# Performance work log

Hardware: AMD Instinct MI355X
Metric: run time of the kernel (lower is better)

Reference implementation:

```python
import jax, jax.numpy as jnp
import numpy as np
import math

HEAD_DIM = 128
N_HEADS = 32
N_KV_HEADS = 8
ROPE_THETA = 10000.0


def _rotate_half(x):
    x1, x2 = jnp.split(x, 2, axis=-1)
    return jnp.concatenate([-x2, x1], axis=-1)


def _rope_cos_sin(position_ids, head_dim, theta):
    # position_ids: [B, S] int
    inv_freq = 1.0 / (theta ** (jnp.arange(0, head_dim, 2, dtype=jnp.float32) / head_dim))
    freqs = position_ids.astype(jnp.float32)[..., None] * inv_freq[None, None, :]  # [B,S,D/2]
    emb = jnp.concatenate([freqs, freqs], axis=-1)  # [B,S,D]
    return jnp.cos(emb), jnp.sin(emb)


def setup_inputs() -> dict:
    key = jax.random.key(0)
    k1, k2, k3, k4, k5 = jax.random.split(key, 5)
    B, S, H = 1, 2048, 4096
    hidden_states = jax.random.normal(k1, (B, S, H), dtype=jnp.float32)
    Wq = jax.random.normal(k2, (N_HEADS * HEAD_DIM, H), dtype=jnp.float32) * (1.0 / math.sqrt(H))
    Wk = jax.random.normal(k3, (N_KV_HEADS * HEAD_DIM, H), dtype=jnp.float32) * (1.0 / math.sqrt(H))
    Wv = jax.random.normal(k4, (N_KV_HEADS * HEAD_DIM, H), dtype=jnp.float32) * (1.0 / math.sqrt(H))
    Wo = jax.random.normal(k5, (H, N_HEADS * HEAD_DIM), dtype=jnp.float32) * (1.0 / math.sqrt(H))
    position_ids = jnp.arange(S, dtype=jnp.int32)[None, :]
    return {"hidden_states": hidden_states, "Wq": Wq, "Wk": Wk, "Wv": Wv, "Wo": Wo,
            "position_ids": position_ids}


def reference(hidden_states, Wq, Wk, Wv, Wo, position_ids):
    B, S, H = hidden_states.shape
    d = HEAD_DIM
    groups = N_HEADS // N_KV_HEADS

    # projections (torch Linear: x @ W^T)
    q = (hidden_states @ Wq.T).reshape(B, S, N_HEADS, d).transpose(0, 2, 1, 3)      # [B,Hq,S,d]
    k = (hidden_states @ Wk.T).reshape(B, S, N_KV_HEADS, d).transpose(0, 2, 1, 3)   # [B,Hk,S,d]
    v = (hidden_states @ Wv.T).reshape(B, S, N_KV_HEADS, d).transpose(0, 2, 1, 3)

    cos, sin = _rope_cos_sin(position_ids, d, ROPE_THETA)  # [B,S,d]
    cos = cos[:, None, :, :]
    sin = sin[:, None, :, :]
    q = q * cos + _rotate_half(q) * sin
    k = k * cos + _rotate_half(k) * sin

    # GQA: repeat kv heads
    k = jnp.repeat(k, groups, axis=1)  # [B,Hq,S,d]
    v = jnp.repeat(v, groups, axis=1)

    scores = jnp.einsum('bhqd,bhkd->bhqk', q, k) / math.sqrt(d)
    causal = jnp.tril(jnp.ones((S, S), dtype=bool))
    scores = jnp.where(causal[None, None], scores, jnp.finfo(jnp.float32).min)
    attn = jax.nn.softmax(scores.astype(jnp.float32), axis=-1).astype(q.dtype)

    out = jnp.einsum('bhqk,bhkd->bhqd', attn, v)        # [B,Hq,S,d]
    out = out.transpose(0, 2, 1, 3).reshape(B, S, N_HEADS * d)
    return out @ Wo.T
```

## Files before the change

### kernel.cpp

```cpp
#include <hip/hip_runtime.h>
#include <hip/hip_bf16.h>
#include <cstdint>
#include <cstddef>

#define S_LEN 2048
#define HID   4096
#define HD    128
#define NH    32
#define NKV   8
#define KVW   (NKV * HD)
#define QKVN  (HID + 2 * KVW)

typedef __bf16 bf16x8_t __attribute__((ext_vector_type(8)));
typedef float  f32x4_t  __attribute__((ext_vector_type(4)));
typedef unsigned short u16x8_t __attribute__((ext_vector_type(8)));

__device__ __forceinline__ unsigned short f2b(float f) {
  unsigned u = __float_as_uint(f);
  u += 0x7FFFu + ((u >> 16) & 1u);
  return (unsigned short)(u >> 16);
}
__device__ __forceinline__ float b2f(unsigned short v) {
  return __uint_as_float(((unsigned)v) << 16);
}
__device__ __forceinline__ void gld_lds16(const void* g, void* l) {
  __builtin_amdgcn_global_load_lds(
      (const __attribute__((address_space(1))) void*)g,
      (__attribute__((address_space(3))) void*)l, 16, 0, 0);
}

__global__ void cvt_kernel(const float* __restrict__ src,
                           unsigned short* __restrict__ dst, int n4) {
  int i = blockIdx.x * blockDim.x + threadIdx.x;
  int stride = gridDim.x * blockDim.x;
  for (; i < n4; i += stride) {
    float4 v = reinterpret_cast<const float4*>(src)[i];
    ushort4 o;
    o.x = f2b(v.x); o.y = f2b(v.y); o.z = f2b(v.z); o.w = f2b(v.w);
    reinterpret_cast<ushort4*>(dst)[i] = o;
  }
}

__global__ void rope_kernel(unsigned short* __restrict__ Q,
                            unsigned short* __restrict__ Kb,
                            const int* __restrict__ pos_ids) {
  const int total = S_LEN * (NH + NKV) * 64;
  int idx = blockIdx.x * blockDim.x + threadIdx.x;
  int stride = gridDim.x * blockDim.x;
  for (; idx < total; idx += stride) {
    int s   = idx / ((NH + NKV) * 64);
    int rem = idx % ((NH + NKV) * 64);
    int hp  = rem >> 6;
    int i   = rem & 63;
    unsigned short* ptr; int W, h;
    if (hp < NH) { ptr = Q;  W = HID; h = hp; }
    else         { ptr = Kb; W = KVW; h = hp - NH; }
    float pos = (float)pos_ids[s];
    float ang = pos * __expf(-(float)i * 0.14391156516f);
    float sn, cs;
    sincosf(ang, &sn, &cs);
    size_t base = (size_t)s * W + (size_t)h * HD + i;
    float lo = b2f(ptr[base]);
    float hi = b2f(ptr[base + 64]);
    ptr[base]      = f2b(lo * cs - hi * sn);
    ptr[base + 64] = f2b(hi * cs + lo * sn);
  }
}

template <int BN, int MODE>
__global__ __launch_bounds__(512, 4) void gemm4p_kernel(
    const unsigned short* __restrict__ A, const unsigned short* __restrict__ B,
    void* __restrict__ C0, void* __restrict__ C1, void* __restrict__ C2,
    int N, int K) {
  constexpr int NFR = BN / 64;
  constexpr int ABYTES = 128 * 128;
  constexpr int TILE_LDS = ABYTES + BN * 128;
  __shared__ char ldsB[2 * TILE_LDS];

  const int tid  = threadIdx.x;
  const int lane = tid & 63;
  const int wid  = tid >> 6;
  const int wm = wid >> 2, wn = wid & 3;
  const int lr = lane & 15, g = lane >> 4;
  const int bm = blockIdx.y * 128;
  const int bn = blockIdx.x * BN;
  const int nk = K >> 6;
  const int ni = nk >> 1;
  const int xr = (lr & 7) << 4;

  auto stage_u = [&](int t, int u) {
    if (t >= nk) return;
    const int riu = tid >> 3;
    const int cbs = ((tid & 7) << 4) ^ ((riu & 7) << 4);
    const char* src;
    if (u < 2)
      src = (const char*)A + ((size_t)(bm + u * 64 + riu) * K + t * 64) * 2 + cbs;
    else
      src = (const char*)B + ((size_t)(bn + (u - 2) * 64 + riu) * K + t * 64) * 2 + cbs;
    gld_lds16(src, ldsB + (t & 1) * TILE_LDS + u * 8192 + tid * 16);
  };

  auto rdA = [&](const char* bb, int m, int k) {
    const int row = wm * 64 + m * 16 + lr;
    return *(const bf16x8_t*)(bb + row * 128 + ((k * 64 + g * 16) ^ xr));
  };
  auto rdB = [&](const char* bb, int n, int k) {
    const int row = wn * (BN / 4) + n * 16 + lr;
    return *(const bf16x8_t*)(bb + ABYTES + row * 128 + ((k * 64 + g * 16) ^ xr));
  };

  for (int t = 0; t < 2; ++t)
    for (int u = 0; u < 2 + NFR; ++u) stage_u(t, u);
  asm volatile("s_waitcnt vmcnt(0)" ::: "memory");
  __builtin_amdgcn_sched_barrier(0);
  __builtin_amdgcn_s_barrier();

  f32x4_t acc[4][NFR];
#pragma unroll
  for (int m = 0; m < 4; ++m)
#pragma unroll
    for (int n = 0; n < NFR; ++n) acc[m][n] = f32x4_t{0.f, 0.f, 0.f, 0.f};

  bf16x8_t bfr[NFR][2], af[2][2];

#define MFMA_BLOCK(MB)                                                        \
  __builtin_amdgcn_s_setprio(1);                                              \
  _Pragma("unroll") for (int m = 0; m < 2; ++m)                               \
    _Pragma("unroll") for (int n = 0; n < NFR; ++n)                           \
      _Pragma("unroll") for (int k = 0; k < 2; ++k)                           \
        acc[(MB) + m][n] = __builtin_amdgcn_mfma_f32_16x16x32_bf16(           \
            af[m][k], bfr[n][k], acc[(MB) + m][n], 0, 0, 0);                  \
  __builtin_amdgcn_s_setprio(0);

#define GATE()                                                                \
  __builtin_amdgcn_s_barrier();                                               \
  asm volatile("s_waitcnt lgkmcnt(0)" ::: "memory");                          \
  __builtin_amdgcn_sched_barrier(0);

#define RD_A2(bb, m0)                                                         \
  _Pragma("unroll") for (int m = 0; m < 2; ++m)                               \
    _Pragma("unroll") for (int k = 0; k < 2; ++k)                             \
      af[m][k] = rdA(bb, (m0) + m, k);

#define RD_B(bb)                                                              \
  _Pragma("unroll") for (int n = 0; n < NFR; ++n)                             \
    _Pragma("unroll") for (int k = 0; k < 2; ++k)                             \
      bfr[n][k] = rdB(bb, n, k);

  for (int i = 0; i < ni; ++i) {
    const char* bE = ldsB;
    const char* bO = ldsB + TILE_LDS;
    const int tO = 2 * i + 1, tE2 = 2 * i + 2, tO2 = 2 * i + 3;
    const bool last = (i == ni - 1);

    RD_B(bE);
    RD_A2(bE, 0);
    if (i > 0) { stage_u(tO, 0); stage_u(tO, 1); }
    GATE(); MFMA_BLOCK(0);
    __builtin_amdgcn_s_barrier();

    RD_A2(bE, 2);
#pragma unroll
    for (int u = 0; u < NFR; ++u) stage_u(tE2, 2 + u);
    GATE(); MFMA_BLOCK(2);
    if (last) { asm volatile("s_waitcnt vmcnt(0)" ::: "memory"); }
    else      { asm volatile("s_waitcnt vmcnt(%0)" :: "n"(NFR) : "memory"); }
    __builtin_amdgcn_sched_barrier(0);
    __builtin_amdgcn_s_barrier();

    RD_B(bO);
    RD_A2(bO, 0);
    stage_u(tE2, 0); stage_u(tE2, 1);
    GATE(); MFMA_BLOCK(0);
    __builtin_amdgcn_s_barrier();

    RD_A2(bO, 2);
#pragma unroll
    for (int u = 0; u < NFR; ++u) stage_u(tO2, 2 + u);
    GATE(); MFMA_BLOCK(2);
    if (!last) { asm volatile("s_waitcnt vmcnt(%0)" :: "n"(NFR) : "memory"); }
    __builtin_amdgcn_sched_barrier(0);
    __builtin_amdgcn_s_barrier();
  }
#undef MFMA_BLOCK
#undef GATE
#undef RD_A2
#undef RD_B

#pragma unroll
  for (int mf = 0; mf < 4; ++mf) {
    const int row0 = bm + wm * 64 + mf * 16 + g * 4;
#pragma unroll
    for (int nf = 0; nf < NFR; ++nf) {
      const int col = bn + wn * (BN / 4) + nf * 16 + lr;
      if constexpr (MODE == 1) {
#pragma unroll
        for (int r = 0; r < 4; ++r)
          ((float*)C0)[(size_t)(row0 + r) * N + col] = acc[mf][nf][r];
      } else {
        if (col < HID) {
#pragma unroll
          for (int r = 0; r < 4; ++r)
            ((unsigned short*)C0)[(size_t)(row0 + r) * HID + col] = f2b(acc[mf][nf][r]);
        } else if (col < HID + KVW) {
#pragma unroll
          for (int r = 0; r < 4; ++r)
            ((unsigned short*)C1)[(size_t)(row0 + r) * KVW + (col - HID)] = f2b(acc[mf][nf][r]);
        } else {
          const int c2 = col - HID - KVW;
          ushort4 w;
          w.x = f2b(acc[mf][nf][0]); w.y = f2b(acc[mf][nf][1]);
          w.z = f2b(acc[mf][nf][2]); w.w = f2b(acc[mf][nf][3]);
          *(ushort4*)(void*)&((unsigned short*)C2)[(size_t)c2 * S_LEN + row0] = w;
        }
      }
    }
  }
}

__global__ __launch_bounds__(256) void attn_kernel(
    const unsigned short* __restrict__ Q, const unsigned short* __restrict__ K,
    const unsigned short* __restrict__ VtG, unsigned short* __restrict__ O) {
  __shared__ unsigned short Kl[64][136];
  __shared__ unsigned short Vt[128][72];
  __shared__ unsigned short Pl[4][16][72];

  const int tid  = threadIdx.x;
  const int lane = tid & 63;
  const int wave = tid >> 6;
  const int h    = blockIdx.y;
  const int kvh  = h >> 2;
  const int pair = blockIdx.x;
  const int lr   = lane & 15;
  const int g    = lane >> 4;
  const int lk8  = g * 8;
  const float scale = 0.08838834764831845f;
  const unsigned short* Vbase = VtG + (size_t)kvh * HD * S_LEN;

  const int ksr = tid >> 4, ksc = (tid & 15) * 8;
  const int vsr = tid >> 3, vsc = (tid & 7) * 8;

  for (int pass = 0; pass < 2; ++pass) {
    const int qb = pass == 0 ? (31 - pair) : pair;
    const int q0 = qb * 64;
    const int qrow = q0 + wave * 16;
    const int nkv = qb + 1;

    bf16x8_t qf[4];
    {
      const unsigned short* qp = Q + (size_t)(qrow + lr) * HID + (size_t)h * HD;
#pragma unroll
      for (int c = 0; c < 4; ++c)
        qf[c] = *(const bf16x8_t*)(const void*)(qp + c * 32 + lk8);
    }
    f32x4_t oacc[8];
#pragma unroll
    for (int c = 0; c < 8; ++c) oacc[c] = f32x4_t{0.f, 0.f, 0.f, 0.f};
    float m_run = -3e38f, l_run = 0.f;

    u16x8_t kr[4], vr[4];
#pragma unroll
    for (int i = 0; i < 4; ++i)
      kr[i] = *(const u16x8_t*)(const void*)(K + (size_t)(ksr + i * 16) * KVW +
                                             (size_t)kvh * HD + ksc);
#pragma unroll
    for (int i = 0; i < 4; ++i)
      vr[i] = *(const u16x8_t*)(const void*)(Vbase + (size_t)(vsr + i * 32) * S_LEN + vsc);

    for (int it = 0; it < nkv; ++it) {
      const int kv0 = it * 64;
      __builtin_amdgcn_s_barrier();
#pragma unroll
      for (int i = 0; i < 4; ++i)
        *(u16x8_t*)(void*)&Kl[ksr + i * 16][ksc] = kr[i];
#pragma unroll
      for (int i = 0; i < 4; ++i)
        *(u16x8_t*)(void*)&Vt[vsr + i * 32][vsc] = vr[i];
      if (it + 1 < nkv) {
        const int kn = kv0 + 64;
#pragma unroll
        for (int i = 0; i < 4; ++i)
          kr[i] = *(const u16x8_t*)(const void*)(K + (size_t)(kn + ksr + i * 16) * KVW +
                                                 (size_t)kvh * HD + ksc);
#pragma unroll
        for (int i = 0; i < 4; ++i)
          vr[i] = *(const u16x8_t*)(const void*)(Vbase + (size_t)(vsr + i * 32) * S_LEN +
                                                 kn + vsc);
      }
      asm volatile("s_waitcnt lgkmcnt(0)" ::: "memory");
      __builtin_amdgcn_sched_barrier(0);
      __builtin_amdgcn_s_barrier();

      f32x4_t sacc[4];
#pragma unroll
      for (int n = 0; n < 4; ++n) sacc[n] = f32x4_t{0.f, 0.f, 0.f, 0.f};
#pragma unroll
      for (int c = 0; c < 4; ++c) {
        bf16x8_t qc = qf[c];
#pragma unroll
        for (int n = 0; n < 4; ++n) {
          bf16x8_t kf = *(const bf16x8_t*)(const void*)&Kl[n * 16 + lr][c * 32 + lk8];
          sacc[n] = __builtin_amdgcn_mfma_f32_16x16x32_bf16(kf, qc, sacc[n], 0, 0, 0);
        }
      }

      const int qg = qrow + lr;
      const bool diag = (it == nkv - 1);
      float p[16];
      float mloc = -3e38f;
#pragma unroll
      for (int n = 0; n < 4; ++n)
#pragma unroll
        for (int r = 0; r < 4; ++r) {
          float x = sacc[n][r] * scale;
          if (diag) {
            int kg = kv0 + n * 16 + g * 4 + r;
            if (kg > qg) x = -3e38f;
          }
          p[n * 4 + r] = x;
          mloc = fmaxf(mloc, x);
        }
      mloc = fmaxf(mloc, __shfl_xor(mloc, 16));
      mloc = fmaxf(mloc, __shfl_xor(mloc, 32));

      if (__any(mloc > m_run + 8.f)) {
        float m_new = fmaxf(m_run, mloc);
        float alpha = __expf(m_run - m_new);
        float a4[4];
#pragma unroll
        for (int r = 0; r < 4; ++r) a4[r] = __shfl(alpha, g * 4 + r);
#pragma unroll
        for (int c = 0; c < 8; ++c)
#pragma unroll
          for (int r = 0; r < 4; ++r) oacc[c][r] *= a4[r];
        l_run *= alpha;
        m_run = m_new;
      }

      float ssum = 0.f;
#pragma unroll
      for (int i = 0; i < 16; ++i) {
        float e = __expf(p[i] - m_run);
        p[i] = e;
        ssum += e;
      }
      ssum += __shfl_xor(ssum, 16);
      ssum += __shfl_xor(ssum, 32);
      l_run += ssum;

#pragma unroll
      for (int n = 0; n < 4; ++n) {
        ushort4 w;
        w.x = f2b(p[n * 4 + 0]); w.y = f2b(p[n * 4 + 1]);
        w.z = f2b(p[n * 4 + 2]); w.w = f2b(p[n * 4 + 3]);
        *(ushort4*)(void*)&Pl[wave][lr][n * 16 + g * 4] = w;
      }

#pragma unroll
      for (int half = 0; half < 2; ++half) {
        bf16x8_t pf = *(const bf16x8_t*)(const void*)&Pl[wave][lr][half * 32 + lk8];
#pragma unroll
        for (int c = 0; c < 8; ++c) {
          bf16x8_t vf = *(const bf16x8_t*)(const void*)&Vt[c * 16 + lr][half * 32 + lk8];
          oacc[c] = __builtin_amdgcn_mfma_f32_16x16x32_bf16(pf, vf, oacc[c], 0, 0, 0);
        }
      }
    }

    float linv[4];
#pragma unroll
    for (int r = 0; r < 4; ++r) linv[r] = 1.f / __shfl(l_run, g * 4 + r);
#pragma unroll
    for (int r = 0; r < 4; ++r) {
      int row = qrow + g * 4 + r;
#pragma unroll
      for (int c = 0; c < 8; ++c)
        O[(size_t)row * HID + (size_t)h * HD + c * 16 + lr] = f2b(oacc[c][r] * linv[r]);
    }
  }
}

extern "C" void kernel_launch(void* const* d_in, const int* in_sizes, int n_in,
                              void* d_out, int out_size, void* d_ws, size_t ws_size,
                              hipStream_t stream) {
  (void)in_sizes; (void)n_in; (void)out_size; (void)ws_size;
  const float* X  = (const float*)d_in[0];
  const float* Wq = (const float*)d_in[1];
  const float* Wk = (const float*)d_in[2];
  const float* Wv = (const float*)d_in[3];
  const float* Wo = (const float*)d_in[4];
  const int*  pos = (const int*)d_in[5];
  float* out = (float*)d_out;

  unsigned short* Xb  = (unsigned short*)d_ws;
  unsigned short* Wqb = Xb  + (size_t)S_LEN * HID;
  unsigned short* Wkb = Wqb + (size_t)HID * HID;
  unsigned short* Wvb = Wkb + (size_t)KVW * HID;
  unsigned short* Wob = Wvb + (size_t)KVW * HID;
  unsigned short* Qb  = Wob + (size_t)HID * HID;
  unsigned short* Kb  = Qb  + (size_t)S_LEN * HID;
  unsigned short* VtB = Kb  + (size_t)S_LEN * KVW;
  unsigned short* AOb = VtB + (size_t)S_LEN * KVW;

  auto cvt = [&](const float* s, unsigned short* d, size_t n) {
    int n4 = (int)(n / 4);
    int grid = (n4 + 255) / 256;
    if (grid > 4096) grid = 4096;
    cvt_kernel<<<grid, 256, 0, stream>>>(s, d, n4);
  };
  cvt(X,  Xb,  (size_t)S_LEN * HID);
  cvt(Wq, Wqb, (size_t)HID * HID);
  cvt(Wk, Wkb, (size_t)KVW * HID);
  cvt(Wv, Wvb, (size_t)KVW * HID);
  cvt(Wo, Wob, (size_t)HID * HID);

  gemm4p_kernel<192, 2><<<dim3(QKVN / 192, S_LEN / 128), 512, 0, stream>>>(
      Xb, Wqb, Qb, Kb, VtB, QKVN, HID);

  rope_kernel<<<2048, 256, 0, stream>>>(Qb, Kb, pos);

  attn_kernel<<<dim3(16, NH), 256, 0, stream>>>(Qb, Kb, VtB, AOb);

  gemm4p_kernel<128, 1><<<dim3(HID / 128, S_LEN / 128), 512, 0, stream>>>(
      AOb, Wob, out, nullptr, nullptr, HID, HID);
}
```

Baseline: 299.2 us.

## Load GEMM B operand directly from global into registers, keep only A in LDS

The GEMM kernel no longer stages the weight (B) tile through LDS. Each wave loads its B fragments straight from global memory into double-buffered registers one k-tile ahead, and only the A tile is staged in LDS with double buffering. The aim is to cut LDS traffic and footprint and simplify the pipeline to one barrier pair per k-tile. In exchange, each wave issues uncoalesced 16-byte global reads of B that are duplicated across the wm waves and use more registers, and the new vmcnt accounting could mis-wait.

```diff
diff --git a/kernel.cpp b/kernel.cpp
--- a/kernel.cpp
+++ b/kernel.cpp
@@ -68,14 +68,12 @@
 }
 
 template <int BN, int MODE>
-__global__ __launch_bounds__(512, 4) void gemm4p_kernel(
+__global__ __launch_bounds__(512, 4) void gemmbd_kernel(
     const unsigned short* __restrict__ A, const unsigned short* __restrict__ B,
     void* __restrict__ C0, void* __restrict__ C1, void* __restrict__ C2,
     int N, int K) {
   constexpr int NFR = BN / 64;
-  constexpr int ABYTES = 128 * 128;
-  constexpr int TILE_LDS = ABYTES + BN * 128;
-  __shared__ char ldsB[2 * TILE_LDS];
+  __shared__ char ldsA[2 * 16384];
 
   const int tid  = threadIdx.x;
   const int lane = tid & 63;
@@ -85,32 +83,36 @@
   const int bm = blockIdx.y * 128;
   const int bn = blockIdx.x * BN;
   const int nk = K >> 6;
-  const int ni = nk >> 1;
   const int xr = (lr & 7) << 4;
 
-  auto stage_u = [&](int t, int u) {
-    if (t >= nk) return;
+  auto stage_a = [&](int t) {
     const int riu = tid >> 3;
     const int cbs = ((tid & 7) << 4) ^ ((riu & 7) << 4);
-    const char* src;
-    if (u < 2)
-      src = (const char*)A + ((size_t)(bm + u * 64 + riu) * K + t * 64) * 2 + cbs;
-    else
-      src = (const char*)B + ((size_t)(bn + (u - 2) * 64 + riu) * K + t * 64) * 2 + cbs;
-    gld_lds16(src, ldsB + (t & 1) * TILE_LDS + u * 8192 + tid * 16);
+#pragma unroll
+    for (int u = 0; u < 2; ++u) {
+      const char* src =
+          (const char*)A + ((size_t)(bm + u * 64 + riu) * K + t * 64) * 2 + cbs;
+      gld_lds16(src, ldsA + (t & 1) * 16384 + u * 8192 + tid * 16);
+    }
   };
 
-  auto rdA = [&](const char* bb, int m, int k) {
+  auto rdA = [&](int t, int m, int k) {
     const int row = wm * 64 + m * 16 + lr;
-    return *(const bf16x8_t*)(bb + row * 128 + ((k * 64 + g * 16) ^ xr));
+    return *(const bf16x8_t*)(ldsA + (t & 1) * 16384 + row * 128 +
+                              ((k * 64 + g * 16) ^ xr));
   };
-  auto rdB = [&](const char* bb, int n, int k) {
-    const int row = wn * (BN / 4) + n * 16 + lr;
-    return *(const bf16x8_t*)(bb + ABYTES + row * 128 + ((k * 64 + g * 16) ^ xr));
-  };
-
-  for (int t = 0; t < 2; ++t)
-    for (int u = 0; u < 2 + NFR; ++u) stage_u(t, u);
+
+#define LD_B(dst, t)                                                          \
+  _Pragma("unroll") for (int n = 0; n < NFR; ++n)                             \
+    _Pragma("unroll") for (int k = 0; k < 2; ++k)                             \
+      dst[n][k] = *(const bf16x8_t*)(const void*)(                            \
+          B + (size_t)(bn + wn * (BN / 4) + n * 16 + lr) * K + (t) * 64 +     \
+          k * 32 + g * 8);
+
+  stage_a(0);
+  if (nk > 1) stage_a(1);
+  bf16x8_t brE[NFR][2], brO[NFR][2];
+  LD_B(brE, 0);
   asm volatile("s_waitcnt vmcnt(0)" ::: "memory");
   __builtin_amdgcn_sched_barrier(0);
   __builtin_amdgcn_s_barrier();
@@ -121,71 +123,39 @@
 #pragma unroll
     for (int n = 0; n < NFR; ++n) acc[m][n] = f32x4_t{0.f, 0.f, 0.f, 0.f};
 
-  bf16x8_t bfr[NFR][2], af[2][2];
-
-#define MFMA_BLOCK(MB)                                                        \
-  __builtin_amdgcn_s_setprio(1);                                              \
-  _Pragma("unroll") for (int m = 0; m < 2; ++m)                               \
-    _Pragma("unroll") for (int n = 0; n < NFR; ++n)                           \
+  bf16x8_t af[4][2];
+
+#define TILE(T, BCUR, BNXT)                                                   \
+  {                                                                           \
+    const int t = (T);                                                        \
+    _Pragma("unroll") for (int m = 0; m < 4; ++m)                             \
       _Pragma("unroll") for (int k = 0; k < 2; ++k)                           \
-        acc[(MB) + m][n] = __builtin_amdgcn_mfma_f32_16x16x32_bf16(           \
-            af[m][k], bfr[n][k], acc[(MB) + m][n], 0, 0, 0);                  \
-  __builtin_amdgcn_s_setprio(0);
-
-#define GATE()                                                                \
-  __builtin_amdgcn_s_barrier();                                               \
-  asm volatile("s_waitcnt lgkmcnt(0)" ::: "memory");                          \
-  __builtin_amdgcn_sched_barrier(0);
-
-#define RD_A2(bb, m0)                                                         \
-  _Pragma("unroll") for (int m = 0; m < 2; ++m)                               \
-    _Pragma("unroll") for (int k = 0; k < 2; ++k)                             \
-      af[m][k] = rdA(bb, (m0) + m, k);
-
-#define RD_B(bb)                                                              \
-  _Pragma("unroll") for (int n = 0; n < NFR; ++n)                             \
-    _Pragma("unroll") for (int k = 0; k < 2; ++k)                             \
-      bfr[n][k] = rdB(bb, n, k);
-
-  for (int i = 0; i < ni; ++i) {
-    const char* bE = ldsB;
-    const char* bO = ldsB + TILE_LDS;
-    const int tO = 2 * i + 1, tE2 = 2 * i + 2, tO2 = 2 * i + 3;
-    const bool last = (i == ni - 1);
-
-    RD_B(bE);
-    RD_A2(bE, 0);
-    if (i > 0) { stage_u(tO, 0); stage_u(tO, 1); }
-    GATE(); MFMA_BLOCK(0);
-    __builtin_amdgcn_s_barrier();
-
-    RD_A2(bE, 2);
-#pragma unroll
-    for (int u = 0; u < NFR; ++u) stage_u(tE2, 2 + u);
-    GATE(); MFMA_BLOCK(2);
-    if (last) { asm volatile("s_waitcnt vmcnt(0)" ::: "memory"); }
-    else      { asm volatile("s_waitcnt vmcnt(%0)" :: "n"(NFR) : "memory"); }
-    __builtin_amdgcn_sched_barrier(0);
-    __builtin_amdgcn_s_barrier();
-
-    RD_B(bO);
-    RD_A2(bO, 0);
-    stage_u(tE2, 0); stage_u(tE2, 1);
-    GATE(); MFMA_BLOCK(0);
-    __builtin_amdgcn_s_barrier();
-
-    RD_A2(bO, 2);
-#pragma unroll
-    for (int u = 0; u < NFR; ++u) stage_u(tO2, 2 + u);
-    GATE(); MFMA_BLOCK(2);
-    if (!last) { asm volatile("s_waitcnt vmcnt(%0)" :: "n"(NFR) : "memory"); }
-    __builtin_amdgcn_sched_barrier(0);
-    __builtin_amdgcn_s_barrier();
-  }
-#undef MFMA_BLOCK
-#undef GATE
-#undef RD_A2
-#undef RD_B
+        af[m][k] = rdA(t, m, k);                                              \
+    if (t + 1 < nk) { LD_B(BNXT, t + 1); }                                    \
+    __builtin_amdgcn_s_setprio(1);                                            \
+    _Pragma("unroll") for (int m = 0; m < 4; ++m)                             \
+      _Pragma("unroll") for (int n = 0; n < NFR; ++n)                         \
+        _Pragma("unroll") for (int k = 0; k < 2; ++k)                         \
+          acc[m][n] = __builtin_amdgcn_mfma_f32_16x16x32_bf16(                \
+              af[m][k], BCUR[n][k], acc[m][n], 0, 0, 0);                      \
+    __builtin_amdgcn_s_setprio(0);                                            \
+    asm volatile("s_waitcnt lgkmcnt(0)" ::: "memory");                        \
+    __builtin_amdgcn_sched_barrier(0);                                        \
+    __builtin_amdgcn_s_barrier();                                             \
+    if (t + 2 < nk) stage_a(t + 2);                                           \
+    if (t + 1 < nk) {                                                         \
+      asm volatile("s_waitcnt vmcnt(2)" ::: "memory");                        \
+    }                                                                         \
+    __builtin_amdgcn_sched_barrier(0);                                        \
+    __builtin_amdgcn_s_barrier();                                             \
+  }
+
+  for (int i = 0; i < (nk >> 1); ++i) {
+    TILE(2 * i,     brE, brO);
+    TILE(2 * i + 1, brO, brE);
+  }
+#undef TILE
+#undef LD_B
 
 #pragma unroll
   for (int mf = 0; mf < 4; ++mf) {
@@ -414,13 +384,13 @@
   cvt(Wv, Wvb, (size_t)KVW * HID);
   cvt(Wo, Wob, (size_t)HID * HID);
 
-  gemm4p_kernel<192, 2><<<dim3(QKVN / 192, S_LEN / 128), 512, 0, stream>>>(
+  gemmbd_kernel<192, 2><<<dim3(QKVN / 192, S_LEN / 128), 512, 0, stream>>>(
       Xb, Wqb, Qb, Kb, VtB, QKVN, HID);
 
   rope_kernel<<<2048, 256, 0, stream>>>(Qb, Kb, pos);
 
   attn_kernel<<<dim3(16, NH), 256, 0, stream>>>(Qb, Kb, VtB, AOb);
 
-  gemm4p_kernel<128, 1><<<dim3(HID / 128, S_LEN / 128), 512, 0, stream>>>(
+  gemmbd_kernel<128, 1><<<dim3(HID / 128, S_LEN / 128), 512, 0, stream>>>(
       AOb, Wob, out, nullptr, nullptr, HID, HID);
 }
```

New measurement: 800.2 us. 167% more time.

## Double-buffer K/V tiles in LDS via direct global-to-LDS loads with XOR swizzle

Applied to the files above, without the earlier changes.

Replaces register-staged K/V prefetch with direct global-to-LDS loads into two LDS buffers, so the next tile streams in while the current one is consumed. Adds an XOR swizzle on LDS columns to avoid bank conflicts and drops the per-iteration register round-trip and one barrier. The cost is twice the LDS for K/V, which may reduce occupancy. It also relies on the gld_lds16 helper being defined elsewhere in the file.

```diff
diff --git a/kernel.cpp b/kernel.cpp
--- a/kernel.cpp
+++ b/kernel.cpp
@@ -221,8 +221,8 @@
 __global__ __launch_bounds__(256) void attn_kernel(
     const unsigned short* __restrict__ Q, const unsigned short* __restrict__ K,
     const unsigned short* __restrict__ VtG, unsigned short* __restrict__ O) {
-  __shared__ unsigned short Kl[64][136];
-  __shared__ unsigned short Vt[128][72];
+  __shared__ char KlB[2][16384];
+  __shared__ char VtB2[2][16384];
   __shared__ unsigned short Pl[4][16][72];
 
   const int tid  = threadIdx.x;
@@ -235,10 +235,37 @@
   const int g    = lane >> 4;
   const int lk8  = g * 8;
   const float scale = 0.08838834764831845f;
-  const unsigned short* Vbase = VtG + (size_t)kvh * HD * S_LEN;
-
-  const int ksr = tid >> 4, ksc = (tid & 15) * 8;
-  const int vsr = tid >> 3, vsc = (tid & 7) * 8;
+
+  auto stageK = [&](int kv0, int buf) {
+#pragma unroll
+    for (int j = 0; j < 4; ++j) {
+      const int row  = j * 16 + (tid >> 4);
+      const int colb = ((tid & 15) << 4) ^ ((row & 15) << 4);
+      const char* src =
+          (const char*)(K + (size_t)(kv0 + row) * KVW + (size_t)kvh * HD) + colb;
+      gld_lds16(src, &KlB[buf][row * 256 + ((tid & 15) << 4)]);
+    }
+  };
+  auto stageV = [&](int kv0, int buf) {
+#pragma unroll
+    for (int j = 0; j < 4; ++j) {
+      const int row  = j * 32 + (tid >> 3);
+      const int colb = ((tid & 7) << 4) ^ ((row & 7) << 4);
+      const char* src =
+          (const char*)(VtG + ((size_t)kvh * HD + row) * S_LEN + kv0) + colb;
+      gld_lds16(src, &VtB2[buf][row * 128 + ((tid & 7) << 4)]);
+    }
+  };
+  auto rdK = [&](int buf, int n, int c) {
+    const int row = n * 16 + lr;
+    return *(const bf16x8_t*)&KlB[buf][row * 256 +
+                                       ((c * 64 + g * 16) ^ ((lr & 15) << 4))];
+  };
+  auto rdV = [&](int buf, int c, int half) {
+    const int row = c * 16 + lr;
+    return *(const bf16x8_t*)&VtB2[buf][row * 128 +
+                                        ((half * 64 + g * 16) ^ ((lr & 7) << 4))];
+  };
 
   for (int pass = 0; pass < 2; ++pass) {
     const int qb = pass == 0 ? (31 - pair) : pair;
@@ -258,38 +285,15 @@
     for (int c = 0; c < 8; ++c) oacc[c] = f32x4_t{0.f, 0.f, 0.f, 0.f};
     float m_run = -3e38f, l_run = 0.f;
 
-    u16x8_t kr[4], vr[4];
-#pragma unroll
-    for (int i = 0; i < 4; ++i)
-      kr[i] = *(const u16x8_t*)(const void*)(K + (size_t)(ksr + i * 16) * KVW +
-                                             (size_t)kvh * HD + ksc);
-#pragma unroll
-    for (int i = 0; i < 4; ++i)
-      vr[i] = *(const u16x8_t*)(const void*)(Vbase + (size_t)(vsr + i * 32) * S_LEN + vsc);
+    stageK(0, 0); stageV(0, 0);
+    asm volatile("s_waitcnt vmcnt(0)" ::: "memory");
+    __builtin_amdgcn_sched_barrier(0);
+    __builtin_amdgcn_s_barrier();
 
     for (int it = 0; it < nkv; ++it) {
       const int kv0 = it * 64;
-      __builtin_amdgcn_s_barrier();
-#pragma unroll
-      for (int i = 0; i < 4; ++i)
-        *(u16x8_t*)(void*)&Kl[ksr + i * 16][ksc] = kr[i];
-#pragma unroll
-      for (int i = 0; i < 4; ++i)
-        *(u16x8_t*)(void*)&Vt[vsr + i * 32][vsc] = vr[i];
-      if (it + 1 < nkv) {
-        const int kn = kv0 + 64;
-#pragma unroll
-        for (int i = 0; i < 4; ++i)
-          kr[i] = *(const u16x8_t*)(const void*)(K + (size_t)(kn + ksr + i * 16) * KVW +
-                                                 (size_t)kvh * HD + ksc);
-#pragma unroll
-        for (int i = 0; i < 4; ++i)
-          vr[i] = *(const u16x8_t*)(const void*)(Vbase + (size_t)(vsr + i * 32) * S_LEN +
-                                                 kn + vsc);
-      }
-      asm volatile("s_waitcnt lgkmcnt(0)" ::: "memory");
-      __builtin_amdgcn_sched_barrier(0);
-      __builtin_amdgcn_s_barrier();
+      const int buf = it & 1;
+      if (it + 1 < nkv) { stageK(kv0 + 64, buf ^ 1); stageV(kv0 + 64, buf ^ 1); }
 
       f32x4_t sacc[4];
 #pragma unroll
@@ -298,10 +302,9 @@
       for (int c = 0; c < 4; ++c) {
         bf16x8_t qc = qf[c];
 #pragma unroll
-        for (int n = 0; n < 4; ++n) {
-          bf16x8_t kf = *(const bf16x8_t*)(const void*)&Kl[n * 16 + lr][c * 32 + lk8];
-          sacc[n] = __builtin_amdgcn_mfma_f32_16x16x32_bf16(kf, qc, sacc[n], 0, 0, 0);
-        }
+        for (int n = 0; n < 4; ++n)
+          sacc[n] = __builtin_amdgcn_mfma_f32_16x16x32_bf16(rdK(buf, n, c), qc,
+                                                            sacc[n], 0, 0, 0);
       }
 
       const int qg = qrow + lr;
@@ -360,11 +363,14 @@
       for (int half = 0; half < 2; ++half) {
         bf16x8_t pf = *(const bf16x8_t*)(const void*)&Pl[wave][lr][half * 32 + lk8];
 #pragma unroll
-        for (int c = 0; c < 8; ++c) {
-          bf16x8_t vf = *(const bf16x8_t*)(const void*)&Vt[c * 16 + lr][half * 32 + lk8];
-          oacc[c] = __builtin_amdgcn_mfma_f32_16x16x32_bf16(pf, vf, oacc[c], 0, 0, 0);
-        }
-      }
+        for (int c = 0; c < 8; ++c)
+          oacc[c] = __builtin_amdgcn_mfma_f32_16x16x32_bf16(pf, rdV(buf, c, half),
+                                                            oacc[c], 0, 0, 0);
+      }
+
+      if (it + 1 < nkv) { asm volatile("s_waitcnt vmcnt(0)" ::: "memory"); }
+      __builtin_amdgcn_sched_barrier(0);
+      __builtin_amdgcn_s_barrier();
     }
 
     float linv[4];
```

New measurement: 293.2 us. 1.02x faster.
